# Performance work log

Measured on AMD Instinct MI355X. Metric: run time of the kernel, lower is better.

## Reference

```python
import jax, jax.numpy as jnp
import numpy as np

A0 = 0.529177249
SIGMA = jnp.array([0.5515909, 1.8886297, 1.3225029, 1.2316629,
                   2.1884933, 1.7750372, 1.3677907, 1.3820058], dtype=jnp.float32)


def celu(x):
    return jax.nn.celu(x, alpha=0.1)


def setup_inputs() -> dict:
    key = jax.random.key(0)
    ks = jax.random.split(key, 24)
    N, n, L, E = 512, 64, 384, 8
    H1, H2, H3 = 160, 128, 96
    s = 0.05
    f32 = jnp.float32
    return {
        "species": jax.random.randint(ks[0], (N, n), 0, E, dtype=jnp.int32),
        "coordinates": 3.0 * jax.random.normal(ks[1], (N, n, 3), dtype=f32),
        "net_charge": jax.random.normal(ks[2], (N,), dtype=f32),
        "aev": jax.random.normal(ks[3], (N, n, L), dtype=f32),
        "chi_W1": s * jax.random.normal(ks[4], (L, H1), dtype=f32),
        "chi_b1": s * jax.random.normal(ks[5], (H1,), dtype=f32),
        "chi_W2": s * jax.random.normal(ks[6], (H1, H2), dtype=f32),
        "chi_b2": s * jax.random.normal(ks[7], (H2,), dtype=f32),
        "chi_W3": s * jax.random.normal(ks[8], (H2, H3), dtype=f32),
        "chi_b3": s * jax.random.normal(ks[9], (H3,), dtype=f32),
        "chi_W4": s * jax.random.normal(ks[10], (H3, 1), dtype=f32),
        "chi_b4": s * jax.random.normal(ks[11], (1,), dtype=f32),
        "W1": s * jax.random.normal(ks[12], (E, L + 2, H1), dtype=f32),
        "b1": s * jax.random.normal(ks[13], (E, H1), dtype=f32),
        "W2": s * jax.random.normal(ks[14], (E, H1, H2), dtype=f32),
        "b2": s * jax.random.normal(ks[15], (E, H2), dtype=f32),
        "W3": s * jax.random.normal(ks[16], (E, H2, H3), dtype=f32),
        "b3": s * jax.random.normal(ks[17], (E, H3), dtype=f32),
        "W4": s * jax.random.normal(ks[18], (E, H3), dtype=f32),
        "b4": s * jax.random.normal(ks[19], (E,), dtype=f32),
    }


def _forward(species, coordinates, net_charge, aev,
             chi_W1, chi_b1, chi_W2, chi_b2, chi_W3, chi_b3, chi_W4, chi_b4,
             W1, b1, W2, b2, W3, b3, W4, b4):
    N, n = species.shape
    aev_flat = aev.reshape(N * n, -1)                       # (A, L)

    # nonzero_batch_dmat: distances in atomic units, eps avoids div-by-zero
    diff = coordinates[:, None, :, :] - coordinates[:, :, None, :]
    dist = jnp.sqrt(jnp.sum(diff * diff, -1) + 1e-16) / A0   # (N, n, n)

    pad = (species != -1).astype(aev.dtype)                  # (N, n)
    pair_mask = pad[:, None, :] * pad[:, :, None]            # (N, n, n)
    num_atoms = pad.sum(axis=1)                              # (N,)
    valid = (species.reshape(-1) != -1)                      # (A,)

    # chi_net: 4-layer MLP (CELU 0.1) + Softplus, masked to valid atoms
    h = celu(aev_flat @ chi_W1 + chi_b1)
    h = celu(h @ chi_W2 + chi_b2)
    h = celu(h @ chi_W3 + chi_b3)
    chi = jax.nn.softplus(h @ chi_W4 + chi_b4)[:, 0]
    chi = jnp.where(valid, chi, 0.0).reshape(N, n)

    chi_sum = chi.sum(axis=-1)
    k_net = 1.0 + jnp.abs(net_charge) / chi_sum
    chi_mean = chi_sum / num_atoms
    k_p = jnp.where(net_charge > 0, k_net, 1.0)
    k_n = jnp.where(net_charge < 0, k_net, 1.0)
    q = (-k_n[:, None] * chi + (k_p * chi_mean)[:, None]) * pad  # (N, n)

    # ESPerf: pairwise erf-screened Coulomb potential
    sig = SIGMA[jnp.clip(species, 0)]                        # (N, n)
    sig_sqsum = sig[:, None, :] ** 2 + sig[:, :, None] ** 2
    sig_sqsum = jnp.maximum(sig_sqsum, 1e-8)
    j_ij = jax.scipy.special.erf(dist / jnp.sqrt(2.0 * sig_sqsum)) / dist
    diag_mask = 1.0 - jnp.eye(n, dtype=dist.dtype)
    esp = (q[:, :, None] * j_ij * pair_mask * diag_mask[None]).sum(axis=-2)  # (N, n)
    coulomb_energy = 0.5 * (q * esp).sum(axis=-1)            # (N,)

    # species-routed expert MLPs over [aev | charge | esp] features
    feat = jnp.concatenate(
        [aev_flat, q.reshape(-1, 1), esp.reshape(-1, 1)], axis=1)  # (A, L+2)
    h1 = celu(jnp.einsum('ad,edh->aeh', feat, W1) + b1)      # (A, E, H1)
    h2 = celu(jnp.einsum('aeh,ehk->aek', h1, W2) + b2)       # (A, E, H2)
    h3 = celu(jnp.einsum('aek,ekm->aem', h2, W3) + b3)       # (A, E, H3)
    out_all = jnp.einsum('aem,em->ae', h3, W4) + b4          # (A, E)

    sp = jnp.clip(species.reshape(-1), 0)
    out = jnp.take_along_axis(out_all, sp[:, None], axis=1)[:, 0]
    out = jnp.where(valid, out, 0.0).reshape(N, n)
    mol_energy = out.sum(axis=1)
    return species, mol_energy + coulomb_energy, q


def reference(species, coordinates, net_charge, aev,
              chi_W1, chi_b1, chi_W2, chi_b2, chi_W3, chi_b3, chi_W4, chi_b4,
              W1, b1, W2, b2, W3, b3, W4, b4):
    return _forward(species, coordinates, net_charge, aev,
                    chi_W1, chi_b1, chi_W2, chi_b2, chi_W3, chi_b3, chi_W4, chi_b4,
                    W1, b1, W2, b2, W3, b3, W4, b4)
```

## Files before the change

kernel.cpp:

```cpp
#include <hip/hip_runtime.h>
#include <math.h>

#define A0_INV (1.0f/0.529177249f)

typedef __bf16 bf16x8 __attribute__((ext_vector_type(8)));
typedef __bf16 bf16x4 __attribute__((ext_vector_type(4)));
typedef float  f32x4  __attribute__((ext_vector_type(4)));

__device__ __constant__ float c_SIGMA[8] = {
    0.5515909f, 1.8886297f, 1.3225029f, 1.2316629f,
    2.1884933f, 1.7750372f, 1.3677907f, 1.3820058f};

__device__ __forceinline__ float celu01(float x) {
    return x > 0.0f ? x : 0.1f * (__expf(x * 10.0f) - 1.0f);
}
__device__ __forceinline__ float softplusf_(float x) {
    return fmaxf(x, 0.0f) + log1pf(__expf(-fabsf(x)));
}
__device__ __forceinline__ __bf16 u16_to_bf16(unsigned short u) {
    __bf16 b; __builtin_memcpy(&b, &u, 2); return b;
}
__device__ __forceinline__ unsigned short f_to_bf16_bits(float f) {
    __bf16 b = (__bf16)f; unsigned short u; __builtin_memcpy(&u, &b, 2); return u;
}

__device__ __forceinline__ void pack_one(int idx, const float* __restrict__ W,
                                         __bf16* __restrict__ Bp,
                                         int K, int OUT, int NT, int KT)
{
    int lane = idx & 63;
    int rest = idx >> 6;
    int kt = rest % KT; rest /= KT;
    int nt = rest % NT;
    int e  = rest / NT;
    int col = nt * 16 + (lane & 15);
    int k0  = kt * 32 + (lane >> 4) * 8;
    bf16x8 o;
#pragma unroll
    for (int j = 0; j < 8; ++j) {
        int k = k0 + j;
        float v = (k < K) ? W[((long)e * K + k) * OUT + col] : 0.0f;
        o[j] = (__bf16)v;
    }
    *((bf16x8*)Bp + idx) = o;
}

__global__ __launch_bounds__(256) void pack_all_kernel(
    const float* __restrict__ cW1, const float* __restrict__ cW2, const float* __restrict__ cW3,
    const float* __restrict__ W1,  const float* __restrict__ W2,  const float* __restrict__ W3,
    __bf16* bp_c1, __bf16* bp_c2, __bf16* bp_c3,
    __bf16* bp_e1, __bf16* bp_e2, __bf16* bp_e3)
{
    int idx = blockIdx.x * 256 + threadIdx.x;
    if      (idx <   7680) pack_one(idx,          cW1, bp_c1, 384, 160, 10, 12);
    else if (idx <  10240) pack_one(idx - 7680,   cW2, bp_c2, 160, 128,  8,  5);
    else if (idx <  11776) pack_one(idx - 10240,  cW3, bp_c3, 128,  96,  6,  4);
    else if (idx <  78336) pack_one(idx - 11776,  W1,  bp_e1, 386, 160, 10, 13);
    else if (idx <  98816) pack_one(idx - 78336,  W2,  bp_e2, 160, 128,  8,  5);
    else if (idx < 111104) pack_one(idx - 98816,  W3,  bp_e3, 128,  96,  6,  4);
}

template<int NT, int KT, int INS, int OUTS, bool CELU>
__device__ __forceinline__ void mlp_layer8(const __bf16* sIn, const bf16x8* __restrict__ Bp,
                                           const float* __restrict__ bias, __bf16* sOut, int tid)
{
    const int lane = tid & 63;
    const int wid  = tid >> 6;
    const int mw   = wid >> 2;
    const int nw   = wid & 3;
    const int r16  = lane & 15;
    const int g    = lane >> 4;
    constexpr int NJ = (NT + 3) / 4;
    f32x4 acc[2][NJ];
#pragma unroll
    for (int mi = 0; mi < 2; ++mi)
#pragma unroll
        for (int j = 0; j < NJ; ++j)
            acc[mi][j] = (f32x4){0.f, 0.f, 0.f, 0.f};

    bf16x8 bcur[NJ], bnxt[NJ];
#pragma unroll
    for (int j = 0; j < NJ; ++j) {
        const int nt = nw + 4 * j;
        if (nt < NT) bcur[j] = Bp[(nt * KT) * 64 + lane];
    }
    for (int kt = 0; kt < KT; ++kt) {
        bf16x8 a[2];
#pragma unroll
        for (int mi = 0; mi < 2; ++mi)
            a[mi] = *(const bf16x8*)(sIn + ((mw * 2 + mi) * 16 + r16) * INS + kt * 32 + g * 8);
        if (kt + 1 < KT) {
#pragma unroll
            for (int j = 0; j < NJ; ++j) {
                const int nt = nw + 4 * j;
                if (nt < NT) bnxt[j] = Bp[(nt * KT + kt + 1) * 64 + lane];
            }
        }
#pragma unroll
        for (int j = 0; j < NJ; ++j) {
            const int nt = nw + 4 * j;
            if (nt < NT) {
#pragma unroll
                for (int mi = 0; mi < 2; ++mi)
                    acc[mi][j] = __builtin_amdgcn_mfma_f32_16x16x32_bf16(a[mi], bcur[j], acc[mi][j], 0, 0, 0);
            }
        }
#pragma unroll
        for (int j = 0; j < NJ; ++j) bcur[j] = bnxt[j];
    }
#pragma unroll
    for (int j = 0; j < NJ; ++j) {
        const int nt = nw + 4 * j;
        if (nt < NT) {
            const float bb = bias[nt * 16 + r16];
#pragma unroll
            for (int mi = 0; mi < 2; ++mi)
#pragma unroll
                for (int r = 0; r < 4; ++r) {
                    float v = acc[mi][j][r] + bb;
                    if (CELU) v = celu01(v);
                    sOut[((mw * 2 + mi) * 16 + g * 4 + r) * OUTS + nt * 16 + r16] = (__bf16)v;
                }
        }
    }
}

__device__ __forceinline__ float l4_dot(const __bf16* __restrict__ h,
                                        const float* __restrict__ w4)
{
    float acc = 0.f;
#pragma unroll
    for (int u8 = 0; u8 < 12; ++u8) {
        bf16x8 hv = *(const bf16x8*)(h + u8 * 8);
        float4 wa = *(const float4*)(w4 + u8 * 8);
        float4 wb = *(const float4*)(w4 + u8 * 8 + 4);
        acc = fmaf((float)hv[0], wa.x, acc);
        acc = fmaf((float)hv[1], wa.y, acc);
        acc = fmaf((float)hv[2], wa.z, acc);
        acc = fmaf((float)hv[3], wa.w, acc);
        acc = fmaf((float)hv[4], wb.x, acc);
        acc = fmaf((float)hv[5], wb.y, acc);
        acc = fmaf((float)hv[6], wb.z, acc);
        acc = fmaf((float)hv[7], wb.w, acc);
    }
    return acc;
}

__global__ __launch_bounds__(512) void chimol_kernel(
    const float* __restrict__ aev, const int* __restrict__ species,
    const float* __restrict__ coords, const float* __restrict__ netq,
    const __bf16* __restrict__ bp1, const __bf16* __restrict__ bp2, const __bf16* __restrict__ bp3,
    const float* __restrict__ b1, const float* __restrict__ b2, const float* __restrict__ b3,
    const float* __restrict__ W4, const float* __restrict__ b4,
    __bf16* __restrict__ aev16,
    int* __restrict__ blockCounts, int* __restrict__ rank,
    float* __restrict__ qv, float* __restrict__ esp, float* __restrict__ coul,
    float* __restrict__ o_species, float* __restrict__ o_q)
{
    __shared__ __align__(16) unsigned char smem[50176 + 21504];
    __shared__ float sChi[64];
    __shared__ float sx[64], sy[64], sz[64], sq[64], ss2[64];
    __shared__ float sEsp[8][64];
    __bf16* sFeat = (__bf16*)smem;
    __bf16* sAct1 = (__bf16*)(smem + 50176);
    __bf16* sAct2 = (__bf16*)smem;
    __bf16* sAct3 = (__bf16*)(smem + 17408);
    const int t = threadIdx.x;
    const int m = blockIdx.x;
    const long base = (long)m * 64;

    if (aev16) {
        for (int i = t; i < 64 * 96; i += 512) {
            int row = i / 96, c4 = (i - row * 96) * 4;
            float4 v = *(const float4*)(aev + (base + row) * 384 + c4);
            bf16x4 o = {(__bf16)v.x, (__bf16)v.y, (__bf16)v.z, (__bf16)v.w};
            *(bf16x4*)(sFeat + row * 392 + c4) = o;
            *(bf16x4*)(aev16 + (base + row) * 384 + c4) = o;
        }
    } else {
        for (int i = t; i < 64 * 96; i += 512) {
            int row = i / 96, c4 = (i - row * 96) * 4;
            float4 v = *(const float4*)(aev + (base + row) * 384 + c4);
            bf16x4 o = {(__bf16)v.x, (__bf16)v.y, (__bf16)v.z, (__bf16)v.w};
            *(bf16x4*)(sFeat + row * 392 + c4) = o;
        }
    }
    __syncthreads();
    mlp_layer8<10, 12, 392, 168, true>(sFeat, (const bf16x8*)bp1, b1, sAct1, t);
    __syncthreads();
    mlp_layer8<8, 5, 168, 136, true>(sAct1, (const bf16x8*)bp2, b2, sAct2, t);
    __syncthreads();
    mlp_layer8<6, 4, 136, 104, true>(sAct2, (const bf16x8*)bp3, b3, sAct3, t);
    __syncthreads();
    if (t < 64) {
        float acc = l4_dot(sAct3 + t * 104, W4);
        float chiv = softplusf_(acc + b4[0]);
        long atom = base + t;
        int s = species[atom];
        if (s == -1) chiv = 0.f;
        sChi[t] = chiv;
        unsigned long long mym = 0;
#pragma unroll
        for (int e = 0; e < 8; ++e) {
            unsigned long long bm = __ballot(s == e);
            if (t == e) blockCounts[m * 8 + e] = (int)__popcll(bm);
            if (s == e) mym = bm;
        }
        if (s >= 0) rank[atom] = (int)__popcll(mym & ((1ull << t) - 1ull));
    }
    __syncthreads();

    const int j = t & 63, grp = t >> 6;
    const int atom = (int)base + j;
    int s = species[atom];
    float pad = (s != -1) ? 1.0f : 0.0f;
    float chij = sChi[j];

    float cs = chij, na = pad;
#pragma unroll
    for (int o = 32; o > 0; o >>= 1) {
        cs += __shfl_xor(cs, o);
        na += __shfl_xor(na, o);
    }
    float qc = netq[m];
    float k_net = 1.0f + fabsf(qc) / cs;
    float chi_mean = cs / na;
    float k_p = (qc > 0.0f) ? k_net : 1.0f;
    float k_n = (qc < 0.0f) ? k_net : 1.0f;
    float qj = (-k_n * chij + k_p * chi_mean) * pad;

    float sg = c_SIGMA[s < 0 ? 0 : s];
    float x = coords[atom * 3 + 0], y = coords[atom * 3 + 1], z = coords[atom * 3 + 2];
    if (grp == 0) { sx[j] = x; sy[j] = y; sz[j] = z; sq[j] = qj; ss2[j] = sg * sg; }
    __syncthreads();

    float s2j = sg * sg;
    float ej = 0.0f;
#pragma unroll
    for (int k = 0; k < 8; ++k) {
        int i = grp * 8 + k;
        if (i == j) continue;
        float dx = sx[i] - x, dy = sy[i] - y, dz = sz[i] - z;
        float d = sqrtf(dx * dx + dy * dy + dz * dz + 1e-16f) * A0_INV;
        float ssum = fmaxf(ss2[i] + s2j, 1e-8f);
        float jij = erff(d * rsqrtf(2.0f * ssum)) / d;
        ej = fmaf(sq[i], jij, ej);
    }
    sEsp[grp][j] = ej;
    __syncthreads();
    if (grp == 0) {
        float e = ((sEsp[0][j] + sEsp[1][j]) + (sEsp[2][j] + sEsp[3][j]))
                + ((sEsp[4][j] + sEsp[5][j]) + (sEsp[6][j] + sEsp[7][j]));
        e *= pad;
        float ce = qj * e;
#pragma unroll
        for (int o = 32; o > 0; o >>= 1) ce += __shfl_xor(ce, o);
        if (j == 0) coul[m] = 0.5f * ce;
        qv[atom] = qj;
        esp[atom] = e;
        o_species[atom] = (float)s;
        o_q[atom] = qj;
    }
}

__global__ void bucket_scan_kernel(int* __restrict__ blockCounts,
                                   int* __restrict__ counts, int* __restrict__ offs,
                                   int* __restrict__ workItems, int* __restrict__ workCount,
                                   int nb)
{
    __shared__ int segSum[8][8];
    __shared__ int tot[8];
    const int tid = threadIdx.x;
    const int seg = tid >> 3, e = tid & 7;
    const int per = (nb + 7) / 8;
    const int b0 = seg * per, b1 = min(b0 + per, nb);
    int run = 0;
    for (int b = b0; b < b1; ++b) run += blockCounts[b * 8 + e];
    segSum[seg][e] = run;
    __syncthreads();
    if (tid < 8) {
        int r = 0;
        for (int s2 = 0; s2 < 8; ++s2) { int c = segSum[s2][tid]; segSum[s2][tid] = r; r += c; }
        tot[tid] = r;
    }
    __syncthreads();
    int runp = segSum[seg][e];
    for (int b = b0; b < b1; ++b) {
        int c = blockCounts[b * 8 + e];
        blockCounts[b * 8 + e] = runp;
        runp += c;
    }
    if (tid == 0) {
        int o = 0;
        for (int i = 0; i < 8; ++i) { offs[i] = o; counts[i] = tot[i]; o += tot[i]; }
        offs[8] = o;
    }
    if (tid < 8) {
        int pos = 0;
        for (int i = 0; i < tid; ++i) pos += (tot[i] + 63) >> 6;
        int nt_e = (tot[tid] + 63) >> 6;
        for (int k = 0; k < nt_e; ++k) workItems[pos + k] = (tid << 20) | (k * 64);
        if (tid == 7) workCount[0] = pos + nt_e;
    }
}

__global__ __launch_bounds__(256) void bucket_fill_kernel(
    const int* __restrict__ species, const int* __restrict__ blockCounts,
    const int* __restrict__ offs, const int* __restrict__ rank,
    int* __restrict__ bidx, float* __restrict__ outat, int A)
{
    int a = blockIdx.x * 256 + threadIdx.x;
    if (a < A) {
        outat[a] = 0.0f;
        int s = species[a];
        if (s >= 0)
            bidx[offs[s] + blockCounts[(a >> 6) * 8 + s] + rank[a]] = a;
    }
}

__device__ __forceinline__ bf16x8 loadA16(const __bf16* __restrict__ aev16,
                                          int atom, int kt, int g)
{
    bf16x8 z = {};
    if (atom < 0) return z;
    return *(const bf16x8*)(aev16 + (long)atom * 384 + kt * 32 + g * 8);
}
__device__ __forceinline__ bf16x8 loadAf(const float* __restrict__ aev,
                                         int atom, int kt, int g)
{
    bf16x8 z = {};
    if (atom < 0) return z;
    const float* p = aev + (long)atom * 384 + kt * 32 + g * 8;
    float4 va = *(const float4*)p, vb = *(const float4*)(p + 4);
    bf16x8 r = {(__bf16)va.x, (__bf16)va.y, (__bf16)va.z, (__bf16)va.w,
                (__bf16)vb.x, (__bf16)vb.y, (__bf16)vb.z, (__bf16)vb.w};
    return r;
}

template<bool HAVE16>
__global__ __launch_bounds__(512, 4) void expert_mfma_kernel(
    const float* __restrict__ aev, const __bf16* __restrict__ aev16,
    const float* __restrict__ qv, const float* __restrict__ esp,
    const __bf16* __restrict__ bp1, const __bf16* __restrict__ bp2, const __bf16* __restrict__ bp3,
    const float* __restrict__ b1, const float* __restrict__ b2, const float* __restrict__ b3,
    const float* __restrict__ W4, const float* __restrict__ b4,
    const int* __restrict__ counts, const int* __restrict__ offs, const int* __restrict__ bidx,
    const int* __restrict__ workItems, const int* __restrict__ workCount,
    float* __restrict__ outat)
{
    const int bid = blockIdx.x;
    if (bid >= workCount[0]) return;
    const int wi = workItems[bid];
    const int e = wi >> 20;
    const int start = wi & 0xFFFFF;
    const int cnt = counts[e];

    __shared__ __align__(16) unsigned char smem[21504 + 17408];
    __shared__ int said[64];
    __shared__ unsigned int sQE[64];
    __bf16* sAct1 = (__bf16*)smem;
    __bf16* sAct2 = (__bf16*)(smem + 21504);
    __bf16* sAct3 = (__bf16*)smem;
    const int t = threadIdx.x;

    if (t < 64) {
        int a_ = (start + t < cnt) ? bidx[offs[e] + start + t] : -1;
        said[t] = a_;
        float q = 0.f, es = 0.f;
        if (a_ >= 0) { q = qv[a_]; es = esp[a_]; }
        sQE[t] = ((unsigned)f_to_bf16_bits(es) << 16) | f_to_bf16_bits(q);
    }
    __syncthreads();

    {
        const int lane = t & 63, wid = t >> 6;
        const int mw = wid >> 2, nw = wid & 3;
        const int r16 = lane & 15, g = lane >> 4;
        const int atom0 = said[(mw * 2 + 0) * 16 + r16];
        const int atom1 = said[(mw * 2 + 1) * 16 + r16];
        const bf16x8* Bp = (const bf16x8*)bp1 + (size_t)e * 10 * 13 * 64;
        constexpr int NJ = 3;
        f32x4 acc[2][NJ];
#pragma unroll
        for (int mi = 0; mi < 2; ++mi)
#pragma unroll
            for (int j = 0; j < NJ; ++j) acc[mi][j] = (f32x4){0.f, 0.f, 0.f, 0.f};

        bf16x8 bcur[NJ], bnxt[NJ];
#pragma unroll
        for (int j = 0; j < NJ; ++j) {
            const int nt = nw + 4 * j;
            if (nt < 10) bcur[j] = Bp[(nt * 13) * 64 + lane];
        }
        bf16x8 a0c = HAVE16 ? loadA16(aev16, atom0, 0, g) : loadAf(aev, atom0, 0, g);
        bf16x8 a1c = HAVE16 ? loadA16(aev16, atom1, 0, g) : loadAf(aev, atom1, 0, g);

        for (int kt = 0; kt < 12; ++kt) {
#pragma unroll
            for (int j = 0; j < NJ; ++j) {
                const int nt = nw + 4 * j;
                if (nt < 10) bnxt[j] = Bp[(nt * 13 + kt + 1) * 64 + lane];
            }
            bf16x8 a0n, a1n;
            if (kt < 11) {
                a0n = HAVE16 ? loadA16(aev16, atom0, kt + 1, g) : loadAf(aev, atom0, kt + 1, g);
                a1n = HAVE16 ? loadA16(aev16, atom1, kt + 1, g) : loadAf(aev, atom1, kt + 1, g);
            }
#pragma unroll
            for (int j = 0; j < NJ; ++j) {
                const int nt = nw + 4 * j;
                if (nt < 10) {
                    acc[0][j] = __builtin_amdgcn_mfma_f32_16x16x32_bf16(a0c, bcur[j], acc[0][j], 0, 0, 0);
                    acc[1][j] = __builtin_amdgcn_mfma_f32_16x16x32_bf16(a1c, bcur[j], acc[1][j], 0, 0, 0);
                }
            }
#pragma unroll
            for (int j = 0; j < NJ; ++j) bcur[j] = bnxt[j];
            if (kt < 11) { a0c = a0n; a1c = a1n; }
        }
        bf16x8 aq0 = {}, aq1 = {};
        if (g == 0) {
            unsigned qe0 = sQE[(mw * 2 + 0) * 16 + r16];
            unsigned qe1 = sQE[(mw * 2 + 1) * 16 + r16];
            aq0[0] = u16_to_bf16((unsigned short)(qe0 & 0xffff));
            aq0[1] = u16_to_bf16((unsigned short)(qe0 >> 16));
            aq1[0] = u16_to_bf16((unsigned short)(qe1 & 0xffff));
            aq1[1] = u16_to_bf16((unsigned short)(qe1 >> 16));
        }
#pragma unroll
        for (int j = 0; j < NJ; ++j) {
            const int nt = nw + 4 * j;
            if (nt < 10) {
                acc[0][j] = __builtin_amdgcn_mfma_f32_16x16x32_bf16(aq0, bcur[j], acc[0][j], 0, 0, 0);
                acc[1][j] = __builtin_amdgcn_mfma_f32_16x16x32_bf16(aq1, bcur[j], acc[1][j], 0, 0, 0);
            }
        }
#pragma unroll
        for (int j = 0; j < NJ; ++j) {
            const int nt = nw + 4 * j;
            if (nt < 10) {
                const float bb = b1[e * 160 + nt * 16 + r16];
#pragma unroll
                for (int mi = 0; mi < 2; ++mi)
#pragma unroll
                    for (int r = 0; r < 4; ++r) {
                        float v = acc[mi][j][r] + bb;
                        v = celu01(v);
                        sAct1[((mw * 2 + mi) * 16 + g * 4 + r) * 168 + nt * 16 + r16] = (__bf16)v;
                    }
            }
        }
    }
    __syncthreads();
    mlp_layer8<8, 5, 168, 136, true>(sAct1, (const bf16x8*)bp2 + (size_t)e * 8 * 5 * 64,
                                     b2 + e * 128, sAct2, t);
    __syncthreads();
    mlp_layer8<6, 4, 136, 104, true>(sAct2, (const bf16x8*)bp3 + (size_t)e * 6 * 4 * 64,
                                     b3 + e * 96, sAct3, t);
    __syncthreads();
    if (t < 64) {
        int atom = said[t];
        if (atom >= 0) {
            float acc = l4_dot(sAct3 + t * 104, W4 + e * 96);
            outat[atom] = acc + b4[e];
        }
    }
}

__global__ __launch_bounds__(64) void energy_kernel(
    const float* __restrict__ outat, const float* __restrict__ coul,
    float* __restrict__ o_energy)
{
    int m = blockIdx.x, t = threadIdx.x;
    float v = outat[m * 64 + t];
#pragma unroll
    for (int o = 32; o > 0; o >>= 1) v += __shfl_xor(v, o);
    if (t == 0) o_energy[m] = v + coul[m];
}

extern "C" void kernel_launch(void* const* d_in, const int* in_sizes, int n_in,
                              void* d_out, int out_size, void* d_ws, size_t ws_size,
                              hipStream_t stream)
{
    const int*   species = (const int*)  d_in[0];
    const float* coords  = (const float*)d_in[1];
    const float* netq    = (const float*)d_in[2];
    const float* aev     = (const float*)d_in[3];
    const float* cW1 = (const float*)d_in[4];
    const float* cb1 = (const float*)d_in[5];
    const float* cW2 = (const float*)d_in[6];
    const float* cb2 = (const float*)d_in[7];
    const float* cW3 = (const float*)d_in[8];
    const float* cb3 = (const float*)d_in[9];
    const float* cW4 = (const float*)d_in[10];
    const float* cb4 = (const float*)d_in[11];
    const float* W1  = (const float*)d_in[12];
    const float* b1  = (const float*)d_in[13];
    const float* W2  = (const float*)d_in[14];
    const float* b2  = (const float*)d_in[15];
    const float* W3  = (const float*)d_in[16];
    const float* b3  = (const float*)d_in[17];
    const float* W4  = (const float*)d_in[18];
    const float* b4  = (const float*)d_in[19];

    const int N = in_sizes[2];
    const int n = in_sizes[0] / N;
    const int A = N * n;
    const int nb64 = A / 64;
    const int maxWork = nb64 + 8;

    float* fbase   = (float*)d_ws;
    float* qv      = fbase;
    float* esp     = fbase + (size_t)A;
    float* outat   = fbase + (size_t)2 * A;
    float* coul    = fbase + (size_t)3 * A;
    int*   counts  = (int*)(coul + N);
    int*   offs    = counts + 8;
    int*   workCount = offs + 9;
    int*   workItems = workCount + 1;
    int*   blockCounts = workItems + maxWork;
    int*   rank    = blockCounts + nb64 * 8;
    int*   bidx    = rank + A;
    uintptr_t p = ((uintptr_t)(bidx + A) + 15) & ~(uintptr_t)15;
    __bf16* bp_c1 = (__bf16*)p; p += (size_t)10 * 12 * 512 * 2;
    __bf16* bp_c2 = (__bf16*)p; p += (size_t)8  * 5  * 512 * 2;
    __bf16* bp_c3 = (__bf16*)p; p += (size_t)6  * 4  * 512 * 2;
    __bf16* bp_e1 = (__bf16*)p; p += (size_t)8 * 10 * 13 * 512 * 2;
    __bf16* bp_e2 = (__bf16*)p; p += (size_t)8 * 8  * 5  * 512 * 2;
    __bf16* bp_e3 = (__bf16*)p; p += (size_t)8 * 6  * 4  * 512 * 2;
    p = (p + 15) & ~(uintptr_t)15;
    __bf16* aev16 = (__bf16*)p;
    size_t need = (p - (uintptr_t)d_ws) + (size_t)A * 384 * 2;
    if (ws_size < need) aev16 = nullptr;

    float* o_species = (float*)d_out;
    float* o_energy  = o_species + A;
    float* o_q       = o_energy + N;

    pack_all_kernel<<<(111104 + 255) / 256, 256, 0, stream>>>(
        cW1, cW2, cW3, W1, W2, W3, bp_c1, bp_c2, bp_c3, bp_e1, bp_e2, bp_e3);

    chimol_kernel<<<nb64, 512, 0, stream>>>(aev, species, coords, netq,
                                            bp_c1, bp_c2, bp_c3,
                                            cb1, cb2, cb3, cW4, cb4,
                                            aev16, blockCounts, rank,
                                            qv, esp, coul, o_species, o_q);
    bucket_scan_kernel<<<1, 64, 0, stream>>>(blockCounts, counts, offs,
                                             workItems, workCount, nb64);
    bucket_fill_kernel<<<(A + 255) / 256, 256, 0, stream>>>(species, blockCounts, offs,
                                                            rank, bidx, outat, A);
    if (aev16)
        expert_mfma_kernel<true><<<maxWork, 512, 0, stream>>>(
            aev, aev16, qv, esp, bp_e1, bp_e2, bp_e3, b1, b2, b3, W4, b4,
            counts, offs, bidx, workItems, workCount, outat);
    else
        expert_mfma_kernel<false><<<maxWork, 512, 0, stream>>>(
            aev, aev16, qv, esp, bp_e1, bp_e2, bp_e3, b1, b2, b3, W4, b4,
            counts, offs, bidx, workItems, workCount, outat);
    energy_kernel<<<N, 64, 0, stream>>>(outat, coul, o_energy);
}
```

Measured before the change: 94.94 us.

## Fuse charge model, global bucketing and expert MLPs into one per-molecule kernel

Replaces the chain of chimol, bucket scan, bucket fill, global expert and energy kernels with one kernel per molecule. Inside that kernel the atoms are sorted by species into 16-row tiles, and the expert MLPs run on those tiles straight from shared memory. The aev is read again as fp32 rather than through a bf16 copy in global memory, and there is no global scatter or gather through workspace. This removes several launches, the global round trips for q/esp/bidx and the aev16 write. The cost is less work per MFMA, since tiles are 16 rows and padding tiles are partly empty, and the expert weights are reloaded by every molecule block.

```diff
diff --git a/kernel.cpp b/kernel.cpp
--- a/kernel.cpp
+++ b/kernel.cpp
@@ -4,7 +4,6 @@
 #define A0_INV (1.0f/0.529177249f)
 
 typedef __bf16 bf16x8 __attribute__((ext_vector_type(8)));
-typedef __bf16 bf16x4 __attribute__((ext_vector_type(4)));
 typedef float  f32x4  __attribute__((ext_vector_type(4)));
 
 __device__ __constant__ float c_SIGMA[8] = {
@@ -60,6 +59,16 @@
     else if (idx < 111104) pack_one(idx - 98816,  W3,  bp_e3, 128,  96,  6,  4);
 }
 
+__device__ __forceinline__ bf16x8 loadAf(const float* __restrict__ aev,
+                                         int atom, int kt, int g)
+{
+    const float* p = aev + (long)atom * 384 + kt * 32 + g * 8;
+    float4 va = *(const float4*)p, vb = *(const float4*)(p + 4);
+    bf16x8 r = {(__bf16)va.x, (__bf16)va.y, (__bf16)va.z, (__bf16)va.w,
+                (__bf16)vb.x, (__bf16)vb.y, (__bf16)vb.z, (__bf16)vb.w};
+    return r;
+}
+
 template<int NT, int KT, int INS, int OUTS, bool CELU>
 __device__ __forceinline__ void mlp_layer8(const __bf16* sIn, const bf16x8* __restrict__ Bp,
                                            const float* __restrict__ bias, __bf16* sOut, int tid)
@@ -121,6 +130,46 @@
                     if (CELU) v = celu01(v);
                     sOut[((mw * 2 + mi) * 16 + g * 4 + r) * OUTS + nt * 16 + r16] = (__bf16)v;
                 }
+        }
+    }
+}
+
+template<int NT, int KT, int INS, int OUTS>
+__device__ __forceinline__ void mlp_tile2(const __bf16* sIn, const bf16x8* __restrict__ Bp,
+                                          const float* __restrict__ bias, __bf16* sOut,
+                                          int lane, int nw2)
+{
+    const int r16 = lane & 15;
+    const int g   = lane >> 4;
+    constexpr int NJ = NT / 2;
+    f32x4 acc[NJ];
+#pragma unroll
+    for (int j = 0; j < NJ; ++j) acc[j] = (f32x4){0.f, 0.f, 0.f, 0.f};
+    bf16x8 bcur[NJ], bnxt[NJ];
+#pragma unroll
+    for (int j = 0; j < NJ; ++j)
+        bcur[j] = Bp[((nw2 + 2 * j) * KT) * 64 + lane];
+    for (int kt = 0; kt < KT; ++kt) {
+        bf16x8 a = *(const bf16x8*)(sIn + r16 * INS + kt * 32 + g * 8);
+        if (kt + 1 < KT) {
+#pragma unroll
+            for (int j = 0; j < NJ; ++j)
+                bnxt[j] = Bp[((nw2 + 2 * j) * KT + kt + 1) * 64 + lane];
+        }
+#pragma unroll
+        for (int j = 0; j < NJ; ++j)
+            acc[j] = __builtin_amdgcn_mfma_f32_16x16x32_bf16(a, bcur[j], acc[j], 0, 0, 0);
+#pragma unroll
+        for (int j = 0; j < NJ; ++j) bcur[j] = bnxt[j];
+    }
+#pragma unroll
+    for (int j = 0; j < NJ; ++j) {
+        const int nt = nw2 + 2 * j;
+        const float bb = bias[nt * 16 + r16];
+#pragma unroll
+        for (int r = 0; r < 4; ++r) {
+            float v = celu01(acc[j][r] + bb);
+            sOut[(g * 4 + r) * OUTS + nt * 16 + r16] = (__bf16)v;
         }
     }
 }
@@ -146,268 +195,102 @@
     return acc;
 }
 
-__global__ __launch_bounds__(512) void chimol_kernel(
+__global__ __launch_bounds__(512, 4) void fused_kernel(
     const float* __restrict__ aev, const int* __restrict__ species,
     const float* __restrict__ coords, const float* __restrict__ netq,
-    const __bf16* __restrict__ bp1, const __bf16* __restrict__ bp2, const __bf16* __restrict__ bp3,
+    const __bf16* __restrict__ bp_c1, const __bf16* __restrict__ bp_c2, const __bf16* __restrict__ bp_c3,
+    const float* __restrict__ cb1, const float* __restrict__ cb2, const float* __restrict__ cb3,
+    const float* __restrict__ cW4, const float* __restrict__ cb4,
+    const __bf16* __restrict__ bp_e1, const __bf16* __restrict__ bp_e2, const __bf16* __restrict__ bp_e3,
     const float* __restrict__ b1, const float* __restrict__ b2, const float* __restrict__ b3,
     const float* __restrict__ W4, const float* __restrict__ b4,
-    __bf16* __restrict__ aev16,
-    int* __restrict__ blockCounts, int* __restrict__ rank,
-    float* __restrict__ qv, float* __restrict__ esp, float* __restrict__ coul,
-    float* __restrict__ o_species, float* __restrict__ o_q)
-{
-    __shared__ __align__(16) unsigned char smem[50176 + 21504];
-    __shared__ float sChi[64];
-    __shared__ float sx[64], sy[64], sz[64], sq[64], ss2[64];
+    float* __restrict__ o_species, float* __restrict__ o_q, float* __restrict__ o_energy)
+{
+    __shared__ __align__(16) unsigned char smem[21504 + 17408];
+    __bf16* Bb = (__bf16*)smem;
+    __bf16* Cc = (__bf16*)(smem + 21504);
+    __shared__ float sx[64], sy[64], sz[64], sqv[64], ss2[64];
     __shared__ float sEsp[8][64];
-    __bf16* sFeat = (__bf16*)smem;
-    __bf16* sAct1 = (__bf16*)(smem + 50176);
-    __bf16* sAct2 = (__bf16*)smem;
-    __bf16* sAct3 = (__bf16*)(smem + 17408);
+    __shared__ float sChi[64], sOut[64];
+    __shared__ float sCoul;
+    __shared__ unsigned sQE[64];
+    __shared__ int sPerm[192];
+    __shared__ int sTileExpert[12];
+    __shared__ int sTileBase[8];
+    __shared__ int sCnt[8];
+    __shared__ int sNT;
+    __shared__ int sSpec[64];
+
     const int t = threadIdx.x;
     const int m = blockIdx.x;
-    const long base = (long)m * 64;
-
-    if (aev16) {
-        for (int i = t; i < 64 * 96; i += 512) {
-            int row = i / 96, c4 = (i - row * 96) * 4;
-            float4 v = *(const float4*)(aev + (base + row) * 384 + c4);
-            bf16x4 o = {(__bf16)v.x, (__bf16)v.y, (__bf16)v.z, (__bf16)v.w};
-            *(bf16x4*)(sFeat + row * 392 + c4) = o;
-            *(bf16x4*)(aev16 + (base + row) * 384 + c4) = o;
-        }
-    } else {
-        for (int i = t; i < 64 * 96; i += 512) {
-            int row = i / 96, c4 = (i - row * 96) * 4;
-            float4 v = *(const float4*)(aev + (base + row) * 384 + c4);
-            bf16x4 o = {(__bf16)v.x, (__bf16)v.y, (__bf16)v.z, (__bf16)v.w};
-            *(bf16x4*)(sFeat + row * 392 + c4) = o;
-        }
-    }
-    __syncthreads();
-    mlp_layer8<10, 12, 392, 168, true>(sFeat, (const bf16x8*)bp1, b1, sAct1, t);
-    __syncthreads();
-    mlp_layer8<8, 5, 168, 136, true>(sAct1, (const bf16x8*)bp2, b2, sAct2, t);
-    __syncthreads();
-    mlp_layer8<6, 4, 136, 104, true>(sAct2, (const bf16x8*)bp3, b3, sAct3, t);
+    const int base = m * 64;
+    const int lane = t & 63, wid = t >> 6;
+    const int r16 = lane & 15, g = lane >> 4;
+
+    if (t >= 64 && t < 256) sPerm[t - 64] = -1;
+    int myrank = 0, s_ = -1;
+    if (t < 64) {
+        s_ = species[base + t];
+        sSpec[t] = s_;
+        o_species[base + t] = (float)s_;
+        unsigned long long mym = 0;
+#pragma unroll
+        for (int e = 0; e < 8; ++e) {
+            unsigned long long bm = __ballot(s_ == e);
+            if (t == e) sCnt[e] = (int)__popcll(bm);
+            if (s_ == e) mym = bm;
+        }
+        myrank = (int)__popcll(mym & ((1ull << t) - 1ull));
+        if (t == 0) {
+            int tb = 0;
+            for (int e = 0; e < 8; ++e) {
+                sTileBase[e] = tb;
+                int tc = (sCnt[e] + 15) >> 4;
+                for (int k = 0; k < tc; ++k) sTileExpert[tb + k] = e;
+                tb += tc;
+            }
+            sNT = tb;
+        }
+    }
     __syncthreads();
     if (t < 64) {
-        float acc = l4_dot(sAct3 + t * 104, W4);
-        float chiv = softplusf_(acc + b4[0]);
-        long atom = base + t;
-        int s = species[atom];
-        if (s == -1) chiv = 0.f;
-        sChi[t] = chiv;
-        unsigned long long mym = 0;
-#pragma unroll
-        for (int e = 0; e < 8; ++e) {
-            unsigned long long bm = __ballot(s == e);
-            if (t == e) blockCounts[m * 8 + e] = (int)__popcll(bm);
-            if (s == e) mym = bm;
-        }
-        if (s >= 0) rank[atom] = (int)__popcll(mym & ((1ull << t) - 1ull));
-    }
-    __syncthreads();
-
-    const int j = t & 63, grp = t >> 6;
-    const int atom = (int)base + j;
-    int s = species[atom];
-    float pad = (s != -1) ? 1.0f : 0.0f;
-    float chij = sChi[j];
-
-    float cs = chij, na = pad;
-#pragma unroll
-    for (int o = 32; o > 0; o >>= 1) {
-        cs += __shfl_xor(cs, o);
-        na += __shfl_xor(na, o);
-    }
-    float qc = netq[m];
-    float k_net = 1.0f + fabsf(qc) / cs;
-    float chi_mean = cs / na;
-    float k_p = (qc > 0.0f) ? k_net : 1.0f;
-    float k_n = (qc < 0.0f) ? k_net : 1.0f;
-    float qj = (-k_n * chij + k_p * chi_mean) * pad;
-
-    float sg = c_SIGMA[s < 0 ? 0 : s];
-    float x = coords[atom * 3 + 0], y = coords[atom * 3 + 1], z = coords[atom * 3 + 2];
-    if (grp == 0) { sx[j] = x; sy[j] = y; sz[j] = z; sq[j] = qj; ss2[j] = sg * sg; }
-    __syncthreads();
-
-    float s2j = sg * sg;
-    float ej = 0.0f;
-#pragma unroll
-    for (int k = 0; k < 8; ++k) {
-        int i = grp * 8 + k;
-        if (i == j) continue;
-        float dx = sx[i] - x, dy = sy[i] - y, dz = sz[i] - z;
-        float d = sqrtf(dx * dx + dy * dy + dz * dz + 1e-16f) * A0_INV;
-        float ssum = fmaxf(ss2[i] + s2j, 1e-8f);
-        float jij = erff(d * rsqrtf(2.0f * ssum)) / d;
-        ej = fmaf(sq[i], jij, ej);
-    }
-    sEsp[grp][j] = ej;
-    __syncthreads();
-    if (grp == 0) {
-        float e = ((sEsp[0][j] + sEsp[1][j]) + (sEsp[2][j] + sEsp[3][j]))
-                + ((sEsp[4][j] + sEsp[5][j]) + (sEsp[6][j] + sEsp[7][j]));
-        e *= pad;
-        float ce = qj * e;
-#pragma unroll
-        for (int o = 32; o > 0; o >>= 1) ce += __shfl_xor(ce, o);
-        if (j == 0) coul[m] = 0.5f * ce;
-        qv[atom] = qj;
-        esp[atom] = e;
-        o_species[atom] = (float)s;
-        o_q[atom] = qj;
-    }
-}
-
-__global__ void bucket_scan_kernel(int* __restrict__ blockCounts,
-                                   int* __restrict__ counts, int* __restrict__ offs,
-                                   int* __restrict__ workItems, int* __restrict__ workCount,
-                                   int nb)
-{
-    __shared__ int segSum[8][8];
-    __shared__ int tot[8];
-    const int tid = threadIdx.x;
-    const int seg = tid >> 3, e = tid & 7;
-    const int per = (nb + 7) / 8;
-    const int b0 = seg * per, b1 = min(b0 + per, nb);
-    int run = 0;
-    for (int b = b0; b < b1; ++b) run += blockCounts[b * 8 + e];
-    segSum[seg][e] = run;
-    __syncthreads();
-    if (tid < 8) {
-        int r = 0;
-        for (int s2 = 0; s2 < 8; ++s2) { int c = segSum[s2][tid]; segSum[s2][tid] = r; r += c; }
-        tot[tid] = r;
-    }
-    __syncthreads();
-    int runp = segSum[seg][e];
-    for (int b = b0; b < b1; ++b) {
-        int c = blockCounts[b * 8 + e];
-        blockCounts[b * 8 + e] = runp;
-        runp += c;
-    }
-    if (tid == 0) {
-        int o = 0;
-        for (int i = 0; i < 8; ++i) { offs[i] = o; counts[i] = tot[i]; o += tot[i]; }
-        offs[8] = o;
-    }
-    if (tid < 8) {
-        int pos = 0;
-        for (int i = 0; i < tid; ++i) pos += (tot[i] + 63) >> 6;
-        int nt_e = (tot[tid] + 63) >> 6;
-        for (int k = 0; k < nt_e; ++k) workItems[pos + k] = (tid << 20) | (k * 64);
-        if (tid == 7) workCount[0] = pos + nt_e;
-    }
-}
-
-__global__ __launch_bounds__(256) void bucket_fill_kernel(
-    const int* __restrict__ species, const int* __restrict__ blockCounts,
-    const int* __restrict__ offs, const int* __restrict__ rank,
-    int* __restrict__ bidx, float* __restrict__ outat, int A)
-{
-    int a = blockIdx.x * 256 + threadIdx.x;
-    if (a < A) {
-        outat[a] = 0.0f;
-        int s = species[a];
-        if (s >= 0)
-            bidx[offs[s] + blockCounts[(a >> 6) * 8 + s] + rank[a]] = a;
-    }
-}
-
-__device__ __forceinline__ bf16x8 loadA16(const __bf16* __restrict__ aev16,
-                                          int atom, int kt, int g)
-{
-    bf16x8 z = {};
-    if (atom < 0) return z;
-    return *(const bf16x8*)(aev16 + (long)atom * 384 + kt * 32 + g * 8);
-}
-__device__ __forceinline__ bf16x8 loadAf(const float* __restrict__ aev,
-                                         int atom, int kt, int g)
-{
-    bf16x8 z = {};
-    if (atom < 0) return z;
-    const float* p = aev + (long)atom * 384 + kt * 32 + g * 8;
-    float4 va = *(const float4*)p, vb = *(const float4*)(p + 4);
-    bf16x8 r = {(__bf16)va.x, (__bf16)va.y, (__bf16)va.z, (__bf16)va.w,
-                (__bf16)vb.x, (__bf16)vb.y, (__bf16)vb.z, (__bf16)vb.w};
-    return r;
-}
-
-template<bool HAVE16>
-__global__ __launch_bounds__(512, 4) void expert_mfma_kernel(
-    const float* __restrict__ aev, const __bf16* __restrict__ aev16,
-    const float* __restrict__ qv, const float* __restrict__ esp,
-    const __bf16* __restrict__ bp1, const __bf16* __restrict__ bp2, const __bf16* __restrict__ bp3,
-    const float* __restrict__ b1, const float* __restrict__ b2, const float* __restrict__ b3,
-    const float* __restrict__ W4, const float* __restrict__ b4,
-    const int* __restrict__ counts, const int* __restrict__ offs, const int* __restrict__ bidx,
-    const int* __restrict__ workItems, const int* __restrict__ workCount,
-    float* __restrict__ outat)
-{
-    const int bid = blockIdx.x;
-    if (bid >= workCount[0]) return;
-    const int wi = workItems[bid];
-    const int e = wi >> 20;
-    const int start = wi & 0xFFFFF;
-    const int cnt = counts[e];
-
-    __shared__ __align__(16) unsigned char smem[21504 + 17408];
-    __shared__ int said[64];
-    __shared__ unsigned int sQE[64];
-    __bf16* sAct1 = (__bf16*)smem;
-    __bf16* sAct2 = (__bf16*)(smem + 21504);
-    __bf16* sAct3 = (__bf16*)smem;
-    const int t = threadIdx.x;
-
-    if (t < 64) {
-        int a_ = (start + t < cnt) ? bidx[offs[e] + start + t] : -1;
-        said[t] = a_;
-        float q = 0.f, es = 0.f;
-        if (a_ >= 0) { q = qv[a_]; es = esp[a_]; }
-        sQE[t] = ((unsigned)f_to_bf16_bits(es) << 16) | f_to_bf16_bits(q);
-    }
-    __syncthreads();
+        sOut[t] = 0.f;
+        if (s_ >= 0) sPerm[sTileBase[s_] * 16 + myrank] = t;
+    }
 
     {
-        const int lane = t & 63, wid = t >> 6;
         const int mw = wid >> 2, nw = wid & 3;
-        const int r16 = lane & 15, g = lane >> 4;
-        const int atom0 = said[(mw * 2 + 0) * 16 + r16];
-        const int atom1 = said[(mw * 2 + 1) * 16 + r16];
-        const bf16x8* Bp = (const bf16x8*)bp1 + (size_t)e * 10 * 13 * 64;
-        constexpr int NJ = 3;
-        f32x4 acc[2][NJ];
+        const int rowA0 = base + (mw * 2 + 0) * 16 + r16;
+        const int rowA1 = base + (mw * 2 + 1) * 16 + r16;
+        const bf16x8* Bp = (const bf16x8*)bp_c1;
+        f32x4 acc[2][3];
 #pragma unroll
         for (int mi = 0; mi < 2; ++mi)
 #pragma unroll
-            for (int j = 0; j < NJ; ++j) acc[mi][j] = (f32x4){0.f, 0.f, 0.f, 0.f};
-
-        bf16x8 bcur[NJ], bnxt[NJ];
-#pragma unroll
-        for (int j = 0; j < NJ; ++j) {
+            for (int j = 0; j < 3; ++j) acc[mi][j] = (f32x4){0.f, 0.f, 0.f, 0.f};
+        bf16x8 bcur[3], bnxt[3];
+#pragma unroll
+        for (int j = 0; j < 3; ++j) {
             const int nt = nw + 4 * j;
-            if (nt < 10) bcur[j] = Bp[(nt * 13) * 64 + lane];
-        }
-        bf16x8 a0c = HAVE16 ? loadA16(aev16, atom0, 0, g) : loadAf(aev, atom0, 0, g);
-        bf16x8 a1c = HAVE16 ? loadA16(aev16, atom1, 0, g) : loadAf(aev, atom1, 0, g);
-
+            if (nt < 10) bcur[j] = Bp[(nt * 12) * 64 + lane];
+        }
+        bf16x8 a0c = loadAf(aev, rowA0, 0, g);
+        bf16x8 a1c = loadAf(aev, rowA1, 0, g);
         for (int kt = 0; kt < 12; ++kt) {
-#pragma unroll
-            for (int j = 0; j < NJ; ++j) {
-                const int nt = nw + 4 * j;
-                if (nt < 10) bnxt[j] = Bp[(nt * 13 + kt + 1) * 64 + lane];
+            if (kt + 1 < 12) {
+#pragma unroll
+                for (int j = 0; j < 3; ++j) {
+                    const int nt = nw + 4 * j;
+                    if (nt < 10) bnxt[j] = Bp[(nt * 12 + kt + 1) * 64 + lane];
+                }
             }
             bf16x8 a0n, a1n;
-            if (kt < 11) {
-                a0n = HAVE16 ? loadA16(aev16, atom0, kt + 1, g) : loadAf(aev, atom0, kt + 1, g);
-                a1n = HAVE16 ? loadA16(aev16, atom1, kt + 1, g) : loadAf(aev, atom1, kt + 1, g);
-            }
-#pragma unroll
-            for (int j = 0; j < NJ; ++j) {
+            if (kt + 1 < 12) {
+                a0n = loadAf(aev, rowA0, kt + 1, g);
+                a1n = loadAf(aev, rowA1, kt + 1, g);
+            }
+#pragma unroll
+            for (int j = 0; j < 3; ++j) {
                 const int nt = nw + 4 * j;
                 if (nt < 10) {
                     acc[0][j] = __builtin_amdgcn_mfma_f32_16x16x32_bf16(a0c, bcur[j], acc[0][j], 0, 0, 0);
@@ -415,67 +298,177 @@
                 }
             }
 #pragma unroll
-            for (int j = 0; j < NJ; ++j) bcur[j] = bnxt[j];
-            if (kt < 11) { a0c = a0n; a1c = a1n; }
-        }
-        bf16x8 aq0 = {}, aq1 = {};
-        if (g == 0) {
-            unsigned qe0 = sQE[(mw * 2 + 0) * 16 + r16];
-            unsigned qe1 = sQE[(mw * 2 + 1) * 16 + r16];
-            aq0[0] = u16_to_bf16((unsigned short)(qe0 & 0xffff));
-            aq0[1] = u16_to_bf16((unsigned short)(qe0 >> 16));
-            aq1[0] = u16_to_bf16((unsigned short)(qe1 & 0xffff));
-            aq1[1] = u16_to_bf16((unsigned short)(qe1 >> 16));
-        }
-#pragma unroll
-        for (int j = 0; j < NJ; ++j) {
+            for (int j = 0; j < 3; ++j) bcur[j] = bnxt[j];
+            if (kt + 1 < 12) { a0c = a0n; a1c = a1n; }
+        }
+#pragma unroll
+        for (int j = 0; j < 3; ++j) {
             const int nt = nw + 4 * j;
             if (nt < 10) {
-                acc[0][j] = __builtin_amdgcn_mfma_f32_16x16x32_bf16(aq0, bcur[j], acc[0][j], 0, 0, 0);
-                acc[1][j] = __builtin_amdgcn_mfma_f32_16x16x32_bf16(aq1, bcur[j], acc[1][j], 0, 0, 0);
-            }
-        }
-#pragma unroll
-        for (int j = 0; j < NJ; ++j) {
-            const int nt = nw + 4 * j;
-            if (nt < 10) {
-                const float bb = b1[e * 160 + nt * 16 + r16];
+                const float bb = cb1[nt * 16 + r16];
 #pragma unroll
                 for (int mi = 0; mi < 2; ++mi)
 #pragma unroll
                     for (int r = 0; r < 4; ++r) {
-                        float v = acc[mi][j][r] + bb;
-                        v = celu01(v);
-                        sAct1[((mw * 2 + mi) * 16 + g * 4 + r) * 168 + nt * 16 + r16] = (__bf16)v;
+                        float v = celu01(acc[mi][j][r] + bb);
+                        Bb[((mw * 2 + mi) * 16 + g * 4 + r) * 168 + nt * 16 + r16] = (__bf16)v;
                     }
             }
         }
     }
     __syncthreads();
-    mlp_layer8<8, 5, 168, 136, true>(sAct1, (const bf16x8*)bp2 + (size_t)e * 8 * 5 * 64,
-                                     b2 + e * 128, sAct2, t);
+    mlp_layer8<8, 5, 168, 136, true>(Bb, (const bf16x8*)bp_c2, cb2, Cc, t);
     __syncthreads();
-    mlp_layer8<6, 4, 136, 104, true>(sAct2, (const bf16x8*)bp3 + (size_t)e * 6 * 4 * 64,
-                                     b3 + e * 96, sAct3, t);
+    mlp_layer8<6, 4, 136, 104, true>(Cc, (const bf16x8*)bp_c3, cb3, Bb, t);
     __syncthreads();
     if (t < 64) {
-        int atom = said[t];
-        if (atom >= 0) {
-            float acc = l4_dot(sAct3 + t * 104, W4 + e * 96);
-            outat[atom] = acc + b4[e];
-        }
-    }
-}
-
-__global__ __launch_bounds__(64) void energy_kernel(
-    const float* __restrict__ outat, const float* __restrict__ coul,
-    float* __restrict__ o_energy)
-{
-    int m = blockIdx.x, t = threadIdx.x;
-    float v = outat[m * 64 + t];
-#pragma unroll
-    for (int o = 32; o > 0; o >>= 1) v += __shfl_xor(v, o);
-    if (t == 0) o_energy[m] = v + coul[m];
+        float acc = l4_dot(Bb + t * 104, cW4);
+        float chiv = softplusf_(acc + cb4[0]);
+        if (s_ == -1) chiv = 0.f;
+        sChi[t] = chiv;
+    }
+    __syncthreads();
+
+    {
+        const int j = lane, grp = wid;
+        const int atom = base + j;
+        int s2 = sSpec[j];
+        float pad = (s2 != -1) ? 1.0f : 0.0f;
+        float chij = sChi[j];
+        float cs = chij, na = pad;
+#pragma unroll
+        for (int o = 32; o > 0; o >>= 1) {
+            cs += __shfl_xor(cs, o);
+            na += __shfl_xor(na, o);
+        }
+        float qc = netq[m];
+        float k_net = 1.0f + fabsf(qc) / cs;
+        float chi_mean = cs / na;
+        float k_p = (qc > 0.0f) ? k_net : 1.0f;
+        float k_n = (qc < 0.0f) ? k_net : 1.0f;
+        float qj = (-k_n * chij + k_p * chi_mean) * pad;
+
+        float sg = c_SIGMA[s2 < 0 ? 0 : s2];
+        float x = coords[atom * 3 + 0], y = coords[atom * 3 + 1], z = coords[atom * 3 + 2];
+        if (grp == 0) { sx[j] = x; sy[j] = y; sz[j] = z; sqv[j] = qj; ss2[j] = sg * sg; }
+        __syncthreads();
+
+        float s2j = sg * sg;
+        float ej = 0.0f;
+#pragma unroll
+        for (int k = 0; k < 8; ++k) {
+            int i = grp * 8 + k;
+            if (i == j) continue;
+            float dx = sx[i] - x, dy = sy[i] - y, dz = sz[i] - z;
+            float d = sqrtf(dx * dx + dy * dy + dz * dz + 1e-16f) * A0_INV;
+            float ssum = fmaxf(ss2[i] + s2j, 1e-8f);
+            float jij = erff(d * rsqrtf(2.0f * ssum)) / d;
+            ej = fmaf(sqv[i], jij, ej);
+        }
+        sEsp[grp][j] = ej;
+        __syncthreads();
+        if (grp == 0) {
+            float e = ((sEsp[0][j] + sEsp[1][j]) + (sEsp[2][j] + sEsp[3][j]))
+                    + ((sEsp[4][j] + sEsp[5][j]) + (sEsp[6][j] + sEsp[7][j]));
+            e *= pad;
+            float ce = qj * e;
+#pragma unroll
+            for (int o = 32; o > 0; o >>= 1) ce += __shfl_xor(ce, o);
+            if (j == 0) sCoul = 0.5f * ce;
+            o_q[atom] = qj;
+            sQE[j] = ((unsigned)f_to_bf16_bits(e) << 16) | f_to_bf16_bits(qj);
+        }
+    }
+    __syncthreads();
+
+    const int nT = sNT;
+    for (int tp = 0; tp * 4 < nT; ++tp) {
+        const int tEnd = min(nT, tp * 4 + 4);
+        const int tloc = wid >> 1, nw2 = wid & 1;
+        const int tileIdx = tp * 4 + tloc;
+        const bool act = tileIdx < tEnd;
+        int e_ = 0, aloc = -1;
+        if (act) {
+            e_ = sTileExpert[tileIdx];
+            aloc = sPerm[tileIdx * 16 + r16];
+        }
+        {
+            f32x4 acc[5];
+#pragma unroll
+            for (int j = 0; j < 5; ++j) acc[j] = (f32x4){0.f, 0.f, 0.f, 0.f};
+            if (act) {
+                const bf16x8* Bp = (const bf16x8*)bp_e1 + (size_t)e_ * 10 * 13 * 64;
+                bf16x8 bcur[5], bnxt[5];
+#pragma unroll
+                for (int j = 0; j < 5; ++j)
+                    bcur[j] = Bp[((nw2 + 2 * j) * 13) * 64 + lane];
+                bf16x8 ac = {};
+                if (aloc >= 0) ac = loadAf(aev, base + aloc, 0, g);
+                for (int kt = 0; kt < 12; ++kt) {
+#pragma unroll
+                    for (int j = 0; j < 5; ++j)
+                        bnxt[j] = Bp[((nw2 + 2 * j) * 13 + kt + 1) * 64 + lane];
+                    bf16x8 an = {};
+                    if (kt + 1 < 12 && aloc >= 0) an = loadAf(aev, base + aloc, kt + 1, g);
+#pragma unroll
+                    for (int j = 0; j < 5; ++j)
+                        acc[j] = __builtin_amdgcn_mfma_f32_16x16x32_bf16(ac, bcur[j], acc[j], 0, 0, 0);
+#pragma unroll
+                    for (int j = 0; j < 5; ++j) bcur[j] = bnxt[j];
+                    ac = an;
+                }
+                bf16x8 aq = {};
+                if (g == 0 && aloc >= 0) {
+                    unsigned qe = sQE[aloc];
+                    aq[0] = u16_to_bf16((unsigned short)(qe & 0xffff));
+                    aq[1] = u16_to_bf16((unsigned short)(qe >> 16));
+                }
+#pragma unroll
+                for (int j = 0; j < 5; ++j)
+                    acc[j] = __builtin_amdgcn_mfma_f32_16x16x32_bf16(aq, bcur[j], acc[j], 0, 0, 0);
+#pragma unroll
+                for (int j = 0; j < 5; ++j) {
+                    const int nt = nw2 + 2 * j;
+                    const float bb = b1[e_ * 160 + nt * 16 + r16];
+#pragma unroll
+                    for (int r = 0; r < 4; ++r) {
+                        float v = celu01(acc[j][r] + bb);
+                        Bb[(tloc * 16 + g * 4 + r) * 168 + nt * 16 + r16] = (__bf16)v;
+                    }
+                }
+            }
+        }
+        __syncthreads();
+        if (act)
+            mlp_tile2<8, 5, 168, 136>(Bb + tloc * 16 * 168,
+                                      (const bf16x8*)bp_e2 + (size_t)e_ * 8 * 5 * 64,
+                                      b2 + e_ * 128, Cc + tloc * 16 * 136, lane, nw2);
+        __syncthreads();
+        if (act)
+            mlp_tile2<6, 4, 136, 104>(Cc + tloc * 16 * 136,
+                                      (const bf16x8*)bp_e3 + (size_t)e_ * 6 * 4 * 64,
+                                      b3 + e_ * 96, Bb + tloc * 16 * 104, lane, nw2);
+        __syncthreads();
+        if (t < 64) {
+            int ti = tp * 4 + (t >> 4);
+            if (ti < tEnd) {
+                int al = sPerm[ti * 16 + (t & 15)];
+                if (al >= 0) {
+                    int ee = sTileExpert[ti];
+                    float acc = l4_dot(Bb + t * 104, W4 + ee * 96);
+                    sOut[al] = acc + b4[ee];
+                }
+            }
+        }
+        __syncthreads();
+    }
+
+    if (t < 64) {
+        float v = sOut[t];
+#pragma unroll
+        for (int o = 32; o > 0; o >>= 1) v += __shfl_xor(v, o);
+        if (t == 0) o_energy[m] = v + sCoul;
+    }
 }
 
 extern "C" void kernel_launch(void* const* d_in, const int* in_sizes, int n_in,
@@ -506,32 +499,14 @@
     const int N = in_sizes[2];
     const int n = in_sizes[0] / N;
     const int A = N * n;
-    const int nb64 = A / 64;
-    const int maxWork = nb64 + 8;
-
-    float* fbase   = (float*)d_ws;
-    float* qv      = fbase;
-    float* esp     = fbase + (size_t)A;
-    float* outat   = fbase + (size_t)2 * A;
-    float* coul    = fbase + (size_t)3 * A;
-    int*   counts  = (int*)(coul + N);
-    int*   offs    = counts + 8;
-    int*   workCount = offs + 9;
-    int*   workItems = workCount + 1;
-    int*   blockCounts = workItems + maxWork;
-    int*   rank    = blockCounts + nb64 * 8;
-    int*   bidx    = rank + A;
-    uintptr_t p = ((uintptr_t)(bidx + A) + 15) & ~(uintptr_t)15;
+
+    uintptr_t p = ((uintptr_t)d_ws + 15) & ~(uintptr_t)15;
     __bf16* bp_c1 = (__bf16*)p; p += (size_t)10 * 12 * 512 * 2;
     __bf16* bp_c2 = (__bf16*)p; p += (size_t)8  * 5  * 512 * 2;
     __bf16* bp_c3 = (__bf16*)p; p += (size_t)6  * 4  * 512 * 2;
     __bf16* bp_e1 = (__bf16*)p; p += (size_t)8 * 10 * 13 * 512 * 2;
     __bf16* bp_e2 = (__bf16*)p; p += (size_t)8 * 8  * 5  * 512 * 2;
     __bf16* bp_e3 = (__bf16*)p; p += (size_t)8 * 6  * 4  * 512 * 2;
-    p = (p + 15) & ~(uintptr_t)15;
-    __bf16* aev16 = (__bf16*)p;
-    size_t need = (p - (uintptr_t)d_ws) + (size_t)A * 384 * 2;
-    if (ws_size < need) aev16 = nullptr;
 
     float* o_species = (float*)d_out;
     float* o_energy  = o_species + A;
@@ -540,22 +515,9 @@
     pack_all_kernel<<<(111104 + 255) / 256, 256, 0, stream>>>(
         cW1, cW2, cW3, W1, W2, W3, bp_c1, bp_c2, bp_c3, bp_e1, bp_e2, bp_e3);
 
-    chimol_kernel<<<nb64, 512, 0, stream>>>(aev, species, coords, netq,
-                                            bp_c1, bp_c2, bp_c3,
-                                            cb1, cb2, cb3, cW4, cb4,
-                                            aev16, blockCounts, rank,
-                                            qv, esp, coul, o_species, o_q);
-    bucket_scan_kernel<<<1, 64, 0, stream>>>(blockCounts, counts, offs,
-                                             workItems, workCount, nb64);
-    bucket_fill_kernel<<<(A + 255) / 256, 256, 0, stream>>>(species, blockCounts, offs,
-                                                            rank, bidx, outat, A);
-    if (aev16)
-        expert_mfma_kernel<true><<<maxWork, 512, 0, stream>>>(
-            aev, aev16, qv, esp, bp_e1, bp_e2, bp_e3, b1, b2, b3, W4, b4,
-            counts, offs, bidx, workItems, workCount, outat);
-    else
-        expert_mfma_kernel<false><<<maxWork, 512, 0, stream>>>(
-            aev, aev16, qv, esp, bp_e1, bp_e2, bp_e3, b1, b2, b3, W4, b4,
-            counts, offs, bidx, workItems, workCount, outat);
-    energy_kernel<<<N, 64, 0, stream>>>(outat, coul, o_energy);
-}
+    fused_kernel<<<N, 512, 0, stream>>>(
+        aev, species, coords, netq,
+        bp_c1, bp_c2, bp_c3, cb1, cb2, cb3, cW4, cb4,
+        bp_e1, bp_e2, bp_e3, b1, b2, b3, W4, b4,
+        o_species, o_q, o_energy);
+}
```

Result: slower. 114.5 us (+20.6%).
